# Optimization experiments

Measured on AMD Instinct MI355X. Metric: run time of the kernel, lower is better.

Reference implementation:

```python
import jax, jax.numpy as jnp
import numpy as np
import math

L, H, P = 16384, 128, 256


def setup_inputs() -> dict:
    key = jax.random.key(0)
    k = jax.random.split(key, 6)
    return {
        "input_sequence": jax.random.normal(k[0], (L, H), dtype=jnp.float32),
        "A_diag": jax.random.uniform(k[1], (P,), dtype=jnp.float32),
        "B": (jax.random.uniform(k[2], (P, H, 2), dtype=jnp.float32) * 2.0 - 1.0) / math.sqrt(H),
        "C": (jax.random.uniform(k[3], (H, P, 2), dtype=jnp.float32) * 2.0 - 1.0) / math.sqrt(P),
        "D": jax.random.normal(k[4], (H,), dtype=jnp.float32),
        "steps": jax.random.uniform(k[5], (P,), dtype=jnp.float32),
    }


def _binop(qi, qj):
    # 2x2 block-diagonal matrix product + affine state propagation, per channel.
    iA, iB, iC, iD, ib1, ib2 = qi
    jA, jB, jC, jD, jb1, jb2 = qj
    return (
        jA * iA + jB * iC,
        jA * iB + jB * iD,
        jC * iA + jD * iC,
        jC * iB + jD * iD,
        jA * ib1 + jB * ib2 + jb1,
        jC * ib1 + jD * ib2 + jb2,
    )


def reference(input_sequence, A_diag, B, C, D, steps):
    # LinOSS-IM discretization (implicit)
    A = jax.nn.relu(A_diag)                      # (P,)
    dt = jax.nn.sigmoid(steps)                   # (P,)
    Bc = B[..., 0] + 1j * B[..., 1]              # (P,H) complex64
    Cc = C[..., 0] + 1j * C[..., 1]              # (H,P) complex64

    Bu = input_sequence @ Bc.T                   # (L,P) complex64

    schur = 1.0 / (1.0 + dt ** 2 * A)
    M11 = 1.0 - dt ** 2 * A * schur
    M12 = -dt * A * schur
    M21 = dt * schur
    M22 = schur

    ones = jnp.ones((input_sequence.shape[0], A.shape[0]), dtype=input_sequence.dtype)
    F1 = M11 * Bu * dt                           # (L,P) complex
    F2 = M21 * Bu * dt

    elems = (M11 * ones, M12 * ones, M21 * ones, M22 * ones, F1, F2)
    _, _, _, _, _, x2 = jax.lax.associative_scan(_binop, elems)  # scan over L

    ys = jnp.real(x2 @ Cc.T)                     # (L,H)
    return ys + input_sequence * D
```

## Files before the change

### kernel.cpp

```cpp
#include <hip/hip_runtime.h>
#include <math.h>

#define L 16384
#define H 128
#define P 256
#define CL 32
#define NCH (L/CL)
#define GS 16
#define NG (NCH/GS)
#define KDIM 512
#define NBU 512

typedef __attribute__((ext_vector_type(8))) short short8;
typedef __attribute__((ext_vector_type(4))) float f32x4;

__device__ inline unsigned short f2bf(float f){
  union { float f; unsigned u; } v; v.f = f;
  unsigned u = v.u;
  u += 0x7fffu + ((u >> 16) & 1u);
  return (unsigned short)(u >> 16);
}
__device__ inline float bf2f(unsigned short s){
  union { unsigned u; float f; } v; v.u = ((unsigned)s) << 16;
  return v.f;
}

struct Params { float M11,M12,M21,M22,s1,s2; };

__device__ inline Params get_params(const float* A_diag, const float* steps, int p){
  float A = A_diag[p]; A = A > 0.f ? A : 0.f;
  float dt = 1.f/(1.f + expf(-steps[p]));
  float schur = 1.f/(1.f + dt*dt*A);
  Params q;
  q.M11 = 1.f - dt*dt*A*schur;
  q.M12 = -dt*A*schur;
  q.M21 = dt*schur;
  q.M22 = schur;
  q.s1 = q.M11*dt;
  q.s2 = q.M21*dt;
  return q;
}

__global__ __launch_bounds__(512) void prep_all(const float* __restrict__ in,
                                                const float* __restrict__ B,
                                                const float* __restrict__ Cw,
                                                unsigned short* __restrict__ inb,
                                                unsigned short* __restrict__ BWswz,
                                                unsigned short* __restrict__ Bswz){
  int gid = blockIdx.x*512 + threadIdx.x;
  const float4* g = (const float4*)in;
  float4 a = g[gid*2], b4 = g[gid*2+1];
  union { short8 s; unsigned short u[8]; } o;
  o.u[0]=f2bf(a.x); o.u[1]=f2bf(a.y); o.u[2]=f2bf(a.z); o.u[3]=f2bf(a.w);
  o.u[4]=f2bf(b4.x); o.u[5]=f2bf(b4.y); o.u[6]=f2bf(b4.z); o.u[7]=f2bf(b4.w);
  ((short8*)inb)[gid] = o.s;
  if (gid < H*NBU){
    int k = gid >> 9, n = gid & 511;
    int p = n & 255, c2 = n >> 8;
    float v = B[((size_t)p*H + k)*2 + c2];
    BWswz[((size_t)(k>>3)*NBU + n)*8 + (k&7)] = f2bf(v);
  }
  if (gid < KDIM*H){
    int k = gid >> 7, n = gid & 127;
    float v = (k < P) ? Cw[((size_t)n*P + k)*2]
                      : -Cw[((size_t)n*P + (k-P))*2 + 1];
    Bswz[((size_t)(k>>3)*H + n)*8 + (k&7)] = f2bf(v);
  }
}

__device__ inline void chunk_bu_to_lds(int c, const short* __restrict__ inb,
                                       const short* __restrict__ BWswz,
                                       unsigned short (*sBu)[NBU+8]){
  int tid = threadIdx.x;
  int lane = tid & 63, w = tid >> 6;
  int ml = lane & 15, quad = lane >> 4;
  int mt = w & 1, ng = w >> 1;
  int lm0 = mt*16;
  const short* aptr = inb + (size_t)(c*CL + lm0 + ml)*H + quad*8;
  short8 av[4];
  #pragma unroll
  for (int ks=0; ks<4; ks++) av[ks] = *(const short8*)(aptr + ks*32);
  f32x4 acc[8];
  #pragma unroll
  for (int t=0;t<8;t++) acc[t] = (f32x4){0.f,0.f,0.f,0.f};
  #pragma unroll
  for (int ks=0; ks<4; ks++){
    #pragma unroll
    for (int t=0;t<8;t++){
      int n0 = (ng*8 + t)*16;
      short8 bv = *(const short8*)(BWswz + ((size_t)(ks*4+quad)*NBU + n0 + ml)*8);
      acc[t] = __builtin_amdgcn_mfma_f32_16x16x32_bf16(av[ks], bv, acc[t], 0, 0, 0);
    }
  }
  #pragma unroll
  for (int t=0;t<8;t++){
    int n = (ng*8+t)*16 + ml;
    #pragma unroll
    for (int r=0;r<4;r++)
      sBu[lm0 + quad*4 + r][n] = f2bf(acc[t][r]);
  }
}

__global__ __launch_bounds__(512) void bu_finals(const short* __restrict__ inb,
                                                 const short* __restrict__ BWswz,
                                                 const float* __restrict__ A_diag,
                                                 const float* __restrict__ steps,
                                                 float* __restrict__ finals){
  __shared__ unsigned short sBu[CL][NBU+8];
  int c = blockIdx.x;
  chunk_bu_to_lds(c, inb, BWswz, sBu);
  __syncthreads();
  int tid = threadIdx.x;
  int p = tid & 255, part = tid >> 8;
  Params q = get_params(A_diag, steps, p);
  float x1=0.f, x2=0.f;
  #pragma unroll
  for (int i=0;i<CL;i++){
    float u = bf2f(sBu[i][part*256 + p]);
    float n1 = q.M11*x1 + q.M12*x2 + q.s1*u;
    float n2 = q.M21*x1 + q.M22*x2 + q.s2*u;
    x1 = n1; x2 = n2;
  }
  ((float2*)finals)[(size_t)(part*NCH + c)*P + p] = make_float2(x1,x2);
}

__global__ __launch_bounds__(512) void group_scan(const float* __restrict__ A_diag,
                                                  const float* __restrict__ steps,
                                                  float* zf,
                                                  float* __restrict__ gfin){
  int tid = threadIdx.x;
  int p = tid & (P-1);
  int part = tid >> 8;
  int g = blockIdx.x;
  Params q = get_params(A_diag, steps, p);
  float a=q.M11, b=q.M12, c=q.M21, d=q.M22;
  #pragma unroll
  for (int s=0;s<5;s++){
    float na=a*a+b*c, nb=a*b+b*d, nc=c*a+d*c, nd=c*b+d*d;
    a=na;b=nb;c=nc;d=nd;
  }
  float2* z2 = (float2*)zf;
  float x1=0.f, x2=0.f;
  #pragma unroll
  for (int i=0;i<GS;i++){
    size_t idx = (size_t)(part*NCH + g*GS + i)*P + p;
    float2 f = z2[idx];
    z2[idx] = make_float2(x1,x2);
    float n1 = a*x1 + b*x2 + f.x;
    float n2 = c*x1 + d*x2 + f.y;
    x1=n1; x2=n2;
  }
  ((float2*)gfin)[(size_t)(part*NG + g)*P + p] = make_float2(x1,x2);
}

__global__ __launch_bounds__(512) void fused_out(const short* __restrict__ inb,
                                                 const short* __restrict__ BWswz,
                                                 const short* __restrict__ Bswz,
                                                 const float* __restrict__ A_diag,
                                                 const float* __restrict__ steps,
                                                 const float* __restrict__ zloc,
                                                 const float* __restrict__ gfin,
                                                 const float* __restrict__ Dv,
                                                 const float* __restrict__ in,
                                                 float* __restrict__ out){
  __shared__ unsigned short sX[CL][KDIM+8];
  int c = blockIdx.x;
  chunk_bu_to_lds(c, inb, BWswz, sX);
  __syncthreads();

  int tid = threadIdx.x;
  {
    int p = tid & 255, part = tid >> 8;
    int g = c >> 4, iw = c & (GS-1);
    Params q = get_params(A_diag, steps, p);
    float a=q.M11, b=q.M12, cc=q.M21, dd=q.M22;
    #pragma unroll
    for (int s=0;s<5;s++){
      float na=a*a+b*cc, nb=a*b+b*dd, nc=cc*a+dd*cc, nd=cc*b+dd*dd;
      a=na;b=nb;cc=nc;dd=nd;
    }
    float sa=1.f, sb=0.f, sc=0.f, sd=1.f;
    {
      float wa=a, wb=b, wc=cc, wd=dd;
      #pragma unroll
      for (int bit=0; bit<4; bit++){
        if ((iw>>bit)&1){
          float na = wa*sa + wb*sc, nb = wa*sb + wb*sd;
          float nc = wc*sa + wd*sc, nd = wc*sb + wd*sd;
          sa=na; sb=nb; sc=nc; sd=nd;
        }
        float qa = wa*wa + wb*wc, qb = wa*wb + wb*wd;
        float qc = wc*wa + wd*wc, qd = wc*wb + wd*wd;
        wa=qa; wb=qb; wc=qc; wd=qd;
      }
    }
    float ga=a, gb=b, gc=cc, gd=dd;
    #pragma unroll
    for (int s=0;s<4;s++){
      float na=ga*ga+gb*gc, nb=ga*gb+gb*gd, nc=gc*ga+gd*gc, nd=gc*gb+gd*gd;
      ga=na;gb=nb;gc=nc;gd=nd;
    }
    float y1=0.f, y2=0.f;
    const float2* Z2 = (const float2*)gfin;
    for (int j=0; j<g; j++){
      float2 z = Z2[(size_t)(part*NG + j)*P + p];
      float n1 = ga*y1 + gb*y2 + z.x;
      float n2 = gc*y1 + gd*y2 + z.y;
      y1=n1; y2=n2;
    }
    float2 zc = ((const float2*)zloc)[(size_t)(part*NCH + c)*P + p];
    float x1 = sa*y1 + sb*y2 + zc.x;
    float x2 = sc*y1 + sd*y2 + zc.y;
    #pragma unroll
    for (int i=0;i<CL;i++){
      float u = bf2f(sX[i][part*256 + p]);
      float n1 = q.M11*x1 + q.M12*x2 + q.s1*u;
      float n2 = q.M21*x1 + q.M22*x2 + q.s2*u;
      x1 = n1; x2 = n2;
      sX[i][part*256 + p] = f2bf(x2);
    }
  }
  __syncthreads();

  int lane = tid & 63, w = tid >> 6;
  int ml = lane & 15, quad = lane >> 4;
  int mt = w & 1;
  int ntb = (w >> 1) * 2;
  f32x4 acc[2];
  acc[0] = (f32x4){0.f,0.f,0.f,0.f};
  acc[1] = (f32x4){0.f,0.f,0.f,0.f};
  for (int ks=0; ks<KDIM/32; ks++){
    short8 av = *(const short8*)&sX[mt*16 + ml][ks*32 + quad*8];
    #pragma unroll
    for (int j=0;j<2;j++){
      short8 bv = *(const short8*)(Bswz + ((size_t)(ks*4+quad)*H + (ntb+j)*16 + ml)*8);
      acc[j] = __builtin_amdgcn_mfma_f32_16x16x32_bf16(av, bv, acc[j], 0, 0, 0);
    }
  }
  #pragma unroll
  for (int j=0;j<2;j++){
    int h = (ntb+j)*16 + ml;
    float dv = Dv[h];
    #pragma unroll
    for (int r=0;r<4;r++){
      int l = c*CL + mt*16 + quad*4 + r;
      out[(size_t)l*H + h] = acc[j][r] + in[(size_t)l*H + h]*dv;
    }
  }
}

extern "C" void kernel_launch(void* const* d_in, const int* in_sizes, int n_in,
                              void* d_out, int out_size, void* d_ws, size_t ws_size,
                              hipStream_t stream) {
  const float* in     = (const float*)d_in[0];
  const float* A_diag = (const float*)d_in[1];
  const float* B      = (const float*)d_in[2];
  const float* Cw     = (const float*)d_in[3];
  const float* Dv     = (const float*)d_in[4];
  const float* steps  = (const float*)d_in[5];
  float* out = (float*)d_out;

  unsigned short* inb  = (unsigned short*)d_ws;
  unsigned short* BWswz= inb + (size_t)L*H;
  unsigned short* Bswz = BWswz + (size_t)H*NBU;
  float* finals = (float*)(Bswz + (size_t)KDIM*H);
  float* gfin   = finals + (size_t)2*NCH*P*2;

  prep_all<<<512, 512, 0, stream>>>(in, B, Cw, inb, BWswz, Bswz);
  bu_finals<<<NCH, 512, 0, stream>>>((const short*)inb, (const short*)BWswz,
                                     A_diag, steps, finals);
  group_scan<<<NG, 512, 0, stream>>>(A_diag, steps, finals, gfin);
  fused_out<<<NCH, 512, 0, stream>>>((const short*)inb, (const short*)BWswz,
                                     (const short*)Bswz, A_diag, steps,
                                     finals, gfin, Dv, in, out);
}
```

Baseline: 105.7 us.

## Fuse four kernels into one cooperative kernel with grid syncs

Replaces the prep, chunk-final, group-scan and output kernels with a single cooperative kernel of 512 blocks that uses grid.sync between phases. Input is converted to bf16 on the fly instead of being staged in a bf16 copy. Bu is computed once and kept in LDS across phases rather than recomputed in the last kernel. The local chunk-prefix is now recomputed per block by a serial loop over earlier chunks in its group instead of being written back by the group scan. This removes launch overhead and redundant GEMM work, at the cost of three grid-wide barriers and the requirement that all 512 blocks of 512 threads be co-resident.

```diff
diff --git a/kernel.cpp b/kernel.cpp
--- a/kernel.cpp
+++ b/kernel.cpp
@@ -1,5 +1,8 @@
 #include <hip/hip_runtime.h>
+#include <hip/hip_cooperative_groups.h>
 #include <math.h>
+
+namespace cg = cooperative_groups;
 
 #define L 16384
 #define H 128
@@ -41,147 +44,119 @@
   return q;
 }
 
-__global__ __launch_bounds__(512) void prep_all(const float* __restrict__ in,
-                                                const float* __restrict__ B,
-                                                const float* __restrict__ Cw,
-                                                unsigned short* __restrict__ inb,
-                                                unsigned short* __restrict__ BWswz,
-                                                unsigned short* __restrict__ Bswz){
-  int gid = blockIdx.x*512 + threadIdx.x;
-  const float4* g = (const float4*)in;
-  float4 a = g[gid*2], b4 = g[gid*2+1];
-  union { short8 s; unsigned short u[8]; } o;
-  o.u[0]=f2bf(a.x); o.u[1]=f2bf(a.y); o.u[2]=f2bf(a.z); o.u[3]=f2bf(a.w);
-  o.u[4]=f2bf(b4.x); o.u[5]=f2bf(b4.y); o.u[6]=f2bf(b4.z); o.u[7]=f2bf(b4.w);
-  ((short8*)inb)[gid] = o.s;
-  if (gid < H*NBU){
-    int k = gid >> 9, n = gid & 511;
-    int p = n & 255, c2 = n >> 8;
-    float v = B[((size_t)p*H + k)*2 + c2];
-    BWswz[((size_t)(k>>3)*NBU + n)*8 + (k&7)] = f2bf(v);
-  }
-  if (gid < KDIM*H){
-    int k = gid >> 7, n = gid & 127;
-    float v = (k < P) ? Cw[((size_t)n*P + k)*2]
-                      : -Cw[((size_t)n*P + (k-P))*2 + 1];
-    Bswz[((size_t)(k>>3)*H + n)*8 + (k&7)] = f2bf(v);
-  }
-}
-
-__device__ inline void chunk_bu_to_lds(int c, const short* __restrict__ inb,
-                                       const short* __restrict__ BWswz,
-                                       unsigned short (*sBu)[NBU+8]){
-  int tid = threadIdx.x;
-  int lane = tid & 63, w = tid >> 6;
-  int ml = lane & 15, quad = lane >> 4;
-  int mt = w & 1, ng = w >> 1;
-  int lm0 = mt*16;
-  const short* aptr = inb + (size_t)(c*CL + lm0 + ml)*H + quad*8;
-  short8 av[4];
-  #pragma unroll
-  for (int ks=0; ks<4; ks++) av[ks] = *(const short8*)(aptr + ks*32);
-  f32x4 acc[8];
-  #pragma unroll
-  for (int t=0;t<8;t++) acc[t] = (f32x4){0.f,0.f,0.f,0.f};
-  #pragma unroll
-  for (int ks=0; ks<4; ks++){
+__global__ __launch_bounds__(512, 4) void linoss_all(
+    const float* __restrict__ in,
+    const float* __restrict__ B,
+    const float* __restrict__ Cw,
+    const float* __restrict__ A_diag,
+    const float* __restrict__ steps,
+    const float* __restrict__ Dv,
+    unsigned short* __restrict__ BWswz,
+    unsigned short* __restrict__ Bswz,
+    float* __restrict__ finals,
+    float* __restrict__ gfin,
+    float* __restrict__ out)
+{
+  __shared__ unsigned short sX[CL][NBU+8];
+  cg::grid_group grid = cg::this_grid();
+  const int c   = blockIdx.x;
+  const int tid = threadIdx.x;
+
+  {
+    int gidx = c*512 + tid;
+    if (gidx < H*NBU){
+      int k = gidx >> 9, n = gidx & 511;
+      int p = n & 255, c2 = n >> 8;
+      float v = B[((size_t)p*H + k)*2 + c2];
+      BWswz[((size_t)(k>>3)*NBU + n)*8 + (k&7)] = f2bf(v);
+    } else if (gidx < 2*H*NBU){
+      int g2 = gidx - H*NBU;
+      int k = g2 >> 7, n = g2 & 127;
+      float v = (k < P) ? Cw[((size_t)n*P + k)*2]
+                        : -Cw[((size_t)n*P + (k-P))*2 + 1];
+      Bswz[((size_t)(k>>3)*H + n)*8 + (k&7)] = f2bf(v);
+    }
+  }
+  grid.sync();
+
+  {
+    int lane = tid & 63, w = tid >> 6;
+    int ml = lane & 15, quad = lane >> 4;
+    int mt = w & 1, ng = w >> 1;
+    int lm0 = mt*16;
+    const float* aptr = in + (size_t)(c*CL + lm0 + ml)*H + quad*8;
+    short8 av[4];
+    #pragma unroll
+    for (int ks=0; ks<4; ks++){
+      float4 f0 = *(const float4*)(aptr + ks*32);
+      float4 f1 = *(const float4*)(aptr + ks*32 + 4);
+      union { short8 s; unsigned short u[8]; } o;
+      o.u[0]=f2bf(f0.x); o.u[1]=f2bf(f0.y); o.u[2]=f2bf(f0.z); o.u[3]=f2bf(f0.w);
+      o.u[4]=f2bf(f1.x); o.u[5]=f2bf(f1.y); o.u[6]=f2bf(f1.z); o.u[7]=f2bf(f1.w);
+      av[ks] = o.s;
+    }
+    f32x4 acc[8];
+    #pragma unroll
+    for (int t=0;t<8;t++) acc[t] = (f32x4){0.f,0.f,0.f,0.f};
+    #pragma unroll
+    for (int ks=0; ks<4; ks++){
+      #pragma unroll
+      for (int t=0;t<8;t++){
+        int n0 = (ng*8 + t)*16;
+        short8 bv = *(const short8*)(BWswz + ((size_t)(ks*4+quad)*NBU + n0 + ml)*8);
+        acc[t] = __builtin_amdgcn_mfma_f32_16x16x32_bf16(av[ks], bv, acc[t], 0, 0, 0);
+      }
+    }
     #pragma unroll
     for (int t=0;t<8;t++){
-      int n0 = (ng*8 + t)*16;
-      short8 bv = *(const short8*)(BWswz + ((size_t)(ks*4+quad)*NBU + n0 + ml)*8);
-      acc[t] = __builtin_amdgcn_mfma_f32_16x16x32_bf16(av[ks], bv, acc[t], 0, 0, 0);
-    }
-  }
-  #pragma unroll
-  for (int t=0;t<8;t++){
-    int n = (ng*8+t)*16 + ml;
-    #pragma unroll
-    for (int r=0;r<4;r++)
-      sBu[lm0 + quad*4 + r][n] = f2bf(acc[t][r]);
-  }
-}
-
-__global__ __launch_bounds__(512) void bu_finals(const short* __restrict__ inb,
-                                                 const short* __restrict__ BWswz,
-                                                 const float* __restrict__ A_diag,
-                                                 const float* __restrict__ steps,
-                                                 float* __restrict__ finals){
-  __shared__ unsigned short sBu[CL][NBU+8];
-  int c = blockIdx.x;
-  chunk_bu_to_lds(c, inb, BWswz, sBu);
+      int n = (ng*8+t)*16 + ml;
+      #pragma unroll
+      for (int r=0;r<4;r++)
+        sX[lm0 + quad*4 + r][n] = f2bf(acc[t][r]);
+    }
+  }
   __syncthreads();
-  int tid = threadIdx.x;
-  int p = tid & 255, part = tid >> 8;
+
+  const int p = tid & 255, part = tid >> 8;
   Params q = get_params(A_diag, steps, p);
-  float x1=0.f, x2=0.f;
-  #pragma unroll
-  for (int i=0;i<CL;i++){
-    float u = bf2f(sBu[i][part*256 + p]);
-    float n1 = q.M11*x1 + q.M12*x2 + q.s1*u;
-    float n2 = q.M21*x1 + q.M22*x2 + q.s2*u;
-    x1 = n1; x2 = n2;
-  }
-  ((float2*)finals)[(size_t)(part*NCH + c)*P + p] = make_float2(x1,x2);
-}
-
-__global__ __launch_bounds__(512) void group_scan(const float* __restrict__ A_diag,
-                                                  const float* __restrict__ steps,
-                                                  float* zf,
-                                                  float* __restrict__ gfin){
-  int tid = threadIdx.x;
-  int p = tid & (P-1);
-  int part = tid >> 8;
-  int g = blockIdx.x;
-  Params q = get_params(A_diag, steps, p);
-  float a=q.M11, b=q.M12, c=q.M21, d=q.M22;
+  float Ta=q.M11, Tb=q.M12, Tc=q.M21, Td=q.M22;
   #pragma unroll
   for (int s=0;s<5;s++){
-    float na=a*a+b*c, nb=a*b+b*d, nc=c*a+d*c, nd=c*b+d*d;
-    a=na;b=nb;c=nc;d=nd;
-  }
-  float2* z2 = (float2*)zf;
-  float x1=0.f, x2=0.f;
-  #pragma unroll
-  for (int i=0;i<GS;i++){
-    size_t idx = (size_t)(part*NCH + g*GS + i)*P + p;
-    float2 f = z2[idx];
-    z2[idx] = make_float2(x1,x2);
-    float n1 = a*x1 + b*x2 + f.x;
-    float n2 = c*x1 + d*x2 + f.y;
-    x1=n1; x2=n2;
-  }
-  ((float2*)gfin)[(size_t)(part*NG + g)*P + p] = make_float2(x1,x2);
-}
-
-__global__ __launch_bounds__(512) void fused_out(const short* __restrict__ inb,
-                                                 const short* __restrict__ BWswz,
-                                                 const short* __restrict__ Bswz,
-                                                 const float* __restrict__ A_diag,
-                                                 const float* __restrict__ steps,
-                                                 const float* __restrict__ zloc,
-                                                 const float* __restrict__ gfin,
-                                                 const float* __restrict__ Dv,
-                                                 const float* __restrict__ in,
-                                                 float* __restrict__ out){
-  __shared__ unsigned short sX[CL][KDIM+8];
-  int c = blockIdx.x;
-  chunk_bu_to_lds(c, inb, BWswz, sX);
-  __syncthreads();
-
-  int tid = threadIdx.x;
-  {
-    int p = tid & 255, part = tid >> 8;
+    float na=Ta*Ta+Tb*Tc, nb=Ta*Tb+Tb*Td, nc=Tc*Ta+Td*Tc, nd=Tc*Tb+Td*Td;
+    Ta=na;Tb=nb;Tc=nc;Td=nd;
+  }
+  {
+    float x1=0.f, x2=0.f;
+    #pragma unroll
+    for (int i=0;i<CL;i++){
+      float u = bf2f(sX[i][part*256 + p]);
+      float n1 = q.M11*x1 + q.M12*x2 + q.s1*u;
+      float n2 = q.M21*x1 + q.M22*x2 + q.s2*u;
+      x1 = n1; x2 = n2;
+    }
+    ((float2*)finals)[(size_t)(part*NCH + c)*P + p] = make_float2(x1,x2);
+  }
+  grid.sync();
+
+  if (c < NG){
+    const float2* f2p = (const float2*)finals;
+    float x1=0.f, x2=0.f;
+    #pragma unroll
+    for (int i=0;i<GS;i++){
+      float2 f = f2p[(size_t)(part*NCH + c*GS + i)*P + p];
+      float n1 = Ta*x1 + Tb*x2 + f.x;
+      float n2 = Tc*x1 + Td*x2 + f.y;
+      x1=n1; x2=n2;
+    }
+    ((float2*)gfin)[(size_t)(part*NG + c)*P + p] = make_float2(x1,x2);
+  }
+  grid.sync();
+
+  {
     int g = c >> 4, iw = c & (GS-1);
-    Params q = get_params(A_diag, steps, p);
-    float a=q.M11, b=q.M12, cc=q.M21, dd=q.M22;
-    #pragma unroll
-    for (int s=0;s<5;s++){
-      float na=a*a+b*cc, nb=a*b+b*dd, nc=cc*a+dd*cc, nd=cc*b+dd*dd;
-      a=na;b=nb;cc=nc;dd=nd;
-    }
     float sa=1.f, sb=0.f, sc=0.f, sd=1.f;
     {
-      float wa=a, wb=b, wc=cc, wd=dd;
+      float wa=Ta, wb=Tb, wc=Tc, wd=Td;
       #pragma unroll
       for (int bit=0; bit<4; bit++){
         if ((iw>>bit)&1){
@@ -194,7 +169,7 @@
         wa=qa; wb=qb; wc=qc; wd=qd;
       }
     }
-    float ga=a, gb=b, gc=cc, gd=dd;
+    float ga=Ta, gb=Tb, gc=Tc, gd=Td;
     #pragma unroll
     for (int s=0;s<4;s++){
       float na=ga*ga+gb*gc, nb=ga*gb+gb*gd, nc=gc*ga+gd*gc, nd=gc*gb+gd*gd;
@@ -208,9 +183,18 @@
       float n2 = gc*y1 + gd*y2 + z.y;
       y1=n1; y2=n2;
     }
-    float2 zc = ((const float2*)zloc)[(size_t)(part*NCH + c)*P + p];
-    float x1 = sa*y1 + sb*y2 + zc.x;
-    float x2 = sc*y1 + sd*y2 + zc.y;
+    float z1=0.f, z2v=0.f;
+    {
+      const float2* f2p = (const float2*)finals;
+      for (int j=0; j<iw; j++){
+        float2 f = f2p[(size_t)(part*NCH + g*GS + j)*P + p];
+        float n1 = Ta*z1 + Tb*z2v + f.x;
+        float n2 = Tc*z1 + Td*z2v + f.y;
+        z1=n1; z2v=n2;
+      }
+    }
+    float x1 = sa*y1 + sb*y2 + z1;
+    float x2 = sc*y1 + sd*y2 + z2v;
     #pragma unroll
     for (int i=0;i<CL;i++){
       float u = bf2f(sX[i][part*256 + p]);
@@ -222,29 +206,31 @@
   }
   __syncthreads();
 
-  int lane = tid & 63, w = tid >> 6;
-  int ml = lane & 15, quad = lane >> 4;
-  int mt = w & 1;
-  int ntb = (w >> 1) * 2;
-  f32x4 acc[2];
-  acc[0] = (f32x4){0.f,0.f,0.f,0.f};
-  acc[1] = (f32x4){0.f,0.f,0.f,0.f};
-  for (int ks=0; ks<KDIM/32; ks++){
-    short8 av = *(const short8*)&sX[mt*16 + ml][ks*32 + quad*8];
+  {
+    int lane = tid & 63, w = tid >> 6;
+    int ml = lane & 15, quad = lane >> 4;
+    int mt = w & 1;
+    int ntb = (w >> 1) * 2;
+    f32x4 acc[2];
+    acc[0] = (f32x4){0.f,0.f,0.f,0.f};
+    acc[1] = (f32x4){0.f,0.f,0.f,0.f};
+    for (int ks=0; ks<KDIM/32; ks++){
+      short8 av = *(const short8*)&sX[mt*16 + ml][ks*32 + quad*8];
+      #pragma unroll
+      for (int j=0;j<2;j++){
+        short8 bv = *(const short8*)(Bswz + ((size_t)(ks*4+quad)*H + (ntb+j)*16 + ml)*8);
+        acc[j] = __builtin_amdgcn_mfma_f32_16x16x32_bf16(av, bv, acc[j], 0, 0, 0);
+      }
+    }
     #pragma unroll
     for (int j=0;j<2;j++){
-      short8 bv = *(const short8*)(Bswz + ((size_t)(ks*4+quad)*H + (ntb+j)*16 + ml)*8);
-      acc[j] = __builtin_amdgcn_mfma_f32_16x16x32_bf16(av, bv, acc[j], 0, 0, 0);
-    }
-  }
-  #pragma unroll
-  for (int j=0;j<2;j++){
-    int h = (ntb+j)*16 + ml;
-    float dv = Dv[h];
-    #pragma unroll
-    for (int r=0;r<4;r++){
-      int l = c*CL + mt*16 + quad*4 + r;
-      out[(size_t)l*H + h] = acc[j][r] + in[(size_t)l*H + h]*dv;
+      int h = (ntb+j)*16 + ml;
+      float dv = Dv[h];
+      #pragma unroll
+      for (int r=0;r<4;r++){
+        int l = c*CL + mt*16 + quad*4 + r;
+        out[(size_t)l*H + h] = acc[j][r] + in[(size_t)l*H + h]*dv;
+      }
     }
   }
 }
@@ -260,17 +246,14 @@
   const float* steps  = (const float*)d_in[5];
   float* out = (float*)d_out;
 
-  unsigned short* inb  = (unsigned short*)d_ws;
-  unsigned short* BWswz= inb + (size_t)L*H;
-  unsigned short* Bswz = BWswz + (size_t)H*NBU;
+  unsigned short* BWswz = (unsigned short*)d_ws;
+  unsigned short* Bswz  = BWswz + (size_t)H*NBU;
   float* finals = (float*)(Bswz + (size_t)KDIM*H);
   float* gfin   = finals + (size_t)2*NCH*P*2;
 
-  prep_all<<<512, 512, 0, stream>>>(in, B, Cw, inb, BWswz, Bswz);
-  bu_finals<<<NCH, 512, 0, stream>>>((const short*)inb, (const short*)BWswz,
-                                     A_diag, steps, finals);
-  group_scan<<<NG, 512, 0, stream>>>(A_diag, steps, finals, gfin);
-  fused_out<<<NCH, 512, 0, stream>>>((const short*)inb, (const short*)BWswz,
-                                     (const short*)Bswz, A_diag, steps,
-                                     finals, gfin, Dv, in, out);
-}
+  void* args[] = { (void*)&in, (void*)&B, (void*)&Cw, (void*)&A_diag, (void*)&steps,
+                   (void*)&Dv, (void*)&BWswz, (void*)&Bswz, (void*)&finals,
+                   (void*)&gfin, (void*)&out };
+  hipLaunchCooperativeKernel((const void*)linoss_all, dim3(NCH), dim3(512),
+                             args, 0, stream);
+}
```

Result: slower. 264.5 us (+150.2%).
